# Kernel optimization log

Measured on AMD Instinct MI355X. Metric: run time of the kernel, lower is better.

The kernel has to match this reference:

```python
import jax, jax.numpy as jnp
import numpy as np

N = 8192
NFEAT = 512
NHID = 256
NCLASS = 40
EDGE_P = 0.002  # ~16 avg degree


def setup_inputs() -> dict:
    key = jax.random.key(0)
    k1, k2, k3, k4 = jax.random.split(key, 4)
    x = jax.random.normal(k1, (N, NFEAT), dtype=jnp.float32)
    # unnormalized binary adjacency without self loops (module adds eye itself)
    adj = (jax.random.uniform(k2, (N, N)) < EDGE_P).astype(jnp.float32)
    # GCNConv weights: torch.rand(in, out) -> uniform[0,1)
    W1 = jax.random.uniform(k3, (NFEAT, NHID), dtype=jnp.float32)
    W2 = jax.random.uniform(k4, (NHID, NCLASS), dtype=jnp.float32)
    return {"x": x, "adj": adj, "W1": W1, "W2": W2}


def reference(x, adj, W1, W2):
    n = adj.shape[0]
    # add self loops: in_adj.to_dense() + eye
    A_hat = adj + jnp.eye(n, dtype=adj.dtype)
    # normalize_adj: D^{-1/2} A_hat D^{-1/2} (diag matmuls == row/col scaling)
    d = A_hat.sum(-1) ** -0.5  # [N]
    norm_adj = d[:, None] * A_hat * d[None, :]
    # conv1: relu(adj @ x @ W1); dropout is identity in eval mode
    h = jax.nn.relu((norm_adj @ x) @ W1)
    # conv2 reuses the same normalized adjacency (only one DGG layer by default)
    h2 = jax.nn.relu((norm_adj @ h) @ W2)
    return jax.nn.log_softmax(h2, axis=-1)
```

## Files before the change

### kernel.cpp

```cpp
#include <hip/hip_runtime.h>
#include <math.h>

#define NV 8192
#define CAP 64

__global__ __launch_bounds__(256) void build_graph(
    const float* __restrict__ adj, int* __restrict__ cols,
    int* __restrict__ rowcount, float* __restrict__ dinv,
    float* __restrict__ diagv) {
  int row = blockIdx.x;
  int t = threadIdx.x;
  __shared__ int cnt;
  __shared__ float sdiag;
  __shared__ float ssum[256];
  if (t == 0) { cnt = 0; sdiag = 0.0f; }
  __syncthreads();
  const float4* arow = (const float4*)(adj + (size_t)row * NV);
  float s = 0.0f;
  for (int i = t; i < NV / 4; i += 256) {
    float4 v = arow[i];
    s += v.x + v.y + v.z + v.w;
    int c0 = i * 4;
    if (v.x != 0.0f) { if (c0 + 0 == row) sdiag = v.x; else { int p = atomicAdd(&cnt, 1); if (p < CAP) cols[(size_t)row * CAP + p] = c0 + 0; } }
    if (v.y != 0.0f) { if (c0 + 1 == row) sdiag = v.y; else { int p = atomicAdd(&cnt, 1); if (p < CAP) cols[(size_t)row * CAP + p] = c0 + 1; } }
    if (v.z != 0.0f) { if (c0 + 2 == row) sdiag = v.z; else { int p = atomicAdd(&cnt, 1); if (p < CAP) cols[(size_t)row * CAP + p] = c0 + 2; } }
    if (v.w != 0.0f) { if (c0 + 3 == row) sdiag = v.w; else { int p = atomicAdd(&cnt, 1); if (p < CAP) cols[(size_t)row * CAP + p] = c0 + 3; } }
  }
  ssum[t] = s;
  __syncthreads();
  for (int off = 128; off > 0; off >>= 1) {
    if (t < off) ssum[t] += ssum[t + off];
    __syncthreads();
  }
  if (t == 0) {
    float deg = ssum[0] + 1.0f;
    dinv[row] = 1.0f / sqrtf(deg);
    diagv[row] = sdiag + 1.0f;
    rowcount[row] = cnt > CAP ? CAP : cnt;
  }
}

__global__ __launch_bounds__(256) void gemm_f32(
    const float* __restrict__ A, const float* __restrict__ B,
    float* __restrict__ C, int M, int K, int Nvalid, int ldb, int ldc) {
  __shared__ float As[16][68];
  __shared__ float Bs[16][64];
  int t = threadIdx.x;
  int bm0 = blockIdx.y * 64;
  int bn0 = blockIdx.x * 64;
  int tx = t & 15, ty = t >> 4;
  int ar = t >> 2;
  int ak = (t & 3) * 4;
  int bk = t >> 4;
  int bn = (t & 15) * 4;
  float acc[4][4] = {};
  for (int k0 = 0; k0 < K; k0 += 16) {
    float4 av = *(const float4*)(A + (size_t)(bm0 + ar) * K + k0 + ak);
    float4 bv;
    int bc = bn0 + bn;
    if (bc + 3 < Nvalid) {
      bv = *(const float4*)(B + (size_t)(k0 + bk) * ldb + bc);
    } else {
      bv.x = (bc + 0 < Nvalid) ? B[(size_t)(k0 + bk) * ldb + bc + 0] : 0.0f;
      bv.y = (bc + 1 < Nvalid) ? B[(size_t)(k0 + bk) * ldb + bc + 1] : 0.0f;
      bv.z = (bc + 2 < Nvalid) ? B[(size_t)(k0 + bk) * ldb + bc + 2] : 0.0f;
      bv.w = (bc + 3 < Nvalid) ? B[(size_t)(k0 + bk) * ldb + bc + 3] : 0.0f;
    }
    As[ak + 0][ar] = av.x;
    As[ak + 1][ar] = av.y;
    As[ak + 2][ar] = av.z;
    As[ak + 3][ar] = av.w;
    *(float4*)(&Bs[bk][bn]) = bv;
    __syncthreads();
#pragma unroll
    for (int kk = 0; kk < 16; kk++) {
      float4 a = *(const float4*)(&As[kk][ty * 4]);
      float4 b = *(const float4*)(&Bs[kk][tx * 4]);
      acc[0][0] += a.x * b.x; acc[0][1] += a.x * b.y; acc[0][2] += a.x * b.z; acc[0][3] += a.x * b.w;
      acc[1][0] += a.y * b.x; acc[1][1] += a.y * b.y; acc[1][2] += a.y * b.z; acc[1][3] += a.y * b.w;
      acc[2][0] += a.z * b.x; acc[2][1] += a.z * b.y; acc[2][2] += a.z * b.z; acc[2][3] += a.z * b.w;
      acc[3][0] += a.w * b.x; acc[3][1] += a.w * b.y; acc[3][2] += a.w * b.z; acc[3][3] += a.w * b.w;
    }
    __syncthreads();
  }
#pragma unroll
  for (int i = 0; i < 4; i++) {
    *(float4*)(C + (size_t)(bm0 + ty * 4 + i) * ldc + bn0 + tx * 4) =
        make_float4(acc[i][0], acc[i][1], acc[i][2], acc[i][3]);
  }
}

__global__ __launch_bounds__(256) void spmm_relu_k(
    const float* __restrict__ Z, const int* __restrict__ cols,
    const int* __restrict__ rowcount, const float* __restrict__ dinv,
    const float* __restrict__ diagv, float* __restrict__ H) {
  int row = blockIdx.x;
  int f = threadIdx.x;
  float di = dinv[row];
  float acc = diagv[row] * di * Z[(size_t)row * 256 + f];
  int cnt = rowcount[row];
  const int* cr = cols + (size_t)row * CAP;
  for (int e = 0; e < cnt; e++) {
    int c = cr[e];
    acc += dinv[c] * Z[(size_t)c * 256 + f];
  }
  H[(size_t)row * 256 + f] = fmaxf(acc * di, 0.0f);
}

__global__ __launch_bounds__(256) void spmm2_lsm_k(
    const float* __restrict__ Z, const int* __restrict__ cols,
    const int* __restrict__ rowcount, const float* __restrict__ dinv,
    const float* __restrict__ diagv, float* __restrict__ out) {
  int lane = threadIdx.x & 63;
  int row = blockIdx.x * 4 + (threadIdx.x >> 6);
  float di = dinv[row];
  float acc = 0.0f;
  if (lane < 40) acc = diagv[row] * di * Z[(size_t)row * 64 + lane];
  int cnt = rowcount[row];
  const int* cr = cols + (size_t)row * CAP;
  for (int e = 0; e < cnt; e++) {
    int c = cr[e];
    if (lane < 40) acc += dinv[c] * Z[(size_t)c * 64 + lane];
  }
  float h2 = (lane < 40) ? fmaxf(acc * di, 0.0f) : -INFINITY;
  float m = h2;
  for (int off = 32; off > 0; off >>= 1) m = fmaxf(m, __shfl_xor(m, off, 64));
  float ex = (lane < 40) ? expf(h2 - m) : 0.0f;
  float s = ex;
  for (int off = 32; off > 0; off >>= 1) s += __shfl_xor(s, off, 64);
  float ls = logf(s);
  if (lane < 40) out[(size_t)row * 40 + lane] = h2 - m - ls;
}

extern "C" void kernel_launch(void* const* d_in, const int* in_sizes, int n_in,
                              void* d_out, int out_size, void* d_ws, size_t ws_size,
                              hipStream_t stream) {
  (void)in_sizes; (void)n_in; (void)out_size; (void)ws_size;
  const float* x   = (const float*)d_in[0];
  const float* adj = (const float*)d_in[1];
  const float* W1  = (const float*)d_in[2];
  const float* W2  = (const float*)d_in[3];
  float* out = (float*)d_out;
  char* ws = (char*)d_ws;

  int*   cols     = (int*)(ws);
  int*   rowcount = (int*)(ws + 2097152);
  float* dinv     = (float*)(ws + 2097152 + 32768);
  float* diagv    = (float*)(ws + 2097152 + 65536);
  float* XW1      = (float*)(ws + 2097152 + 98304);
  float* H        = (float*)(ws + 2097152 + 98304 + 8388608);
  float* HW2      = (float*)(ws + 2097152 + 98304 + 16777216);

  hipLaunchKernelGGL(build_graph, dim3(NV), dim3(256), 0, stream,
                     adj, cols, rowcount, dinv, diagv);
  hipLaunchKernelGGL(gemm_f32, dim3(4, 128), dim3(256), 0, stream,
                     x, W1, XW1, NV, 512, 256, 256, 256);
  hipLaunchKernelGGL(spmm_relu_k, dim3(NV), dim3(256), 0, stream,
                     XW1, cols, rowcount, dinv, diagv, H);
  hipLaunchKernelGGL(gemm_f32, dim3(1, 128), dim3(256), 0, stream,
                     H, W2, HW2, NV, 256, 40, 40, 64);
  hipLaunchKernelGGL(spmm2_lsm_k, dim3(NV / 4), dim3(256), 0, stream,
                     HW2, cols, rowcount, dinv, diagv, out);
}
```

Measured before the change: 473.7 us.

## Use wave ballot compaction in graph build and vectorize SpMM gathers

The graph-build kernel replaces per-element shared atomics with wave-level ballot/popcount compaction and counts nonzeros as integers instead of a float tree reduction. It assumes a binary adjacency, so the diagonal value becomes 2 or 1. The first SpMM now processes one row per wave with float4 loads and a 4-way unrolled gather, and the second SpMM gets the same unroll with the lane<40 predicate removed. The aim is to cut atomic contention in the dominant adjacency scan and raise memory-level parallelism in the gathers. The cost is a binary-adjacency assumption and reads of padding columns of HW2.

```diff
diff --git a/kernel.cpp b/kernel.cpp
--- a/kernel.cpp
+++ b/kernel.cpp
@@ -10,32 +10,48 @@
     float* __restrict__ diagv) {
   int row = blockIdx.x;
   int t = threadIdx.x;
+  int lane = t & 63;
   __shared__ int cnt;
-  __shared__ float sdiag;
-  __shared__ float ssum[256];
-  if (t == 0) { cnt = 0; sdiag = 0.0f; }
+  __shared__ int diag_nz;
+  __shared__ int wsum[4];
+  if (t == 0) { cnt = 0; diag_nz = 0; }
   __syncthreads();
   const float4* arow = (const float4*)(adj + (size_t)row * NV);
-  float s = 0.0f;
+  int mycount = 0;
   for (int i = t; i < NV / 4; i += 256) {
     float4 v = arow[i];
-    s += v.x + v.y + v.z + v.w;
-    int c0 = i * 4;
-    if (v.x != 0.0f) { if (c0 + 0 == row) sdiag = v.x; else { int p = atomicAdd(&cnt, 1); if (p < CAP) cols[(size_t)row * CAP + p] = c0 + 0; } }
-    if (v.y != 0.0f) { if (c0 + 1 == row) sdiag = v.y; else { int p = atomicAdd(&cnt, 1); if (p < CAP) cols[(size_t)row * CAP + p] = c0 + 1; } }
-    if (v.z != 0.0f) { if (c0 + 2 == row) sdiag = v.z; else { int p = atomicAdd(&cnt, 1); if (p < CAP) cols[(size_t)row * CAP + p] = c0 + 2; } }
-    if (v.w != 0.0f) { if (c0 + 3 == row) sdiag = v.w; else { int p = atomicAdd(&cnt, 1); if (p < CAP) cols[(size_t)row * CAP + p] = c0 + 3; } }
-  }
-  ssum[t] = s;
+    float va[4] = {v.x, v.y, v.z, v.w};
+#pragma unroll
+    for (int j = 0; j < 4; j++) {
+      bool nz = (va[j] != 0.0f);
+      mycount += nz ? 1 : 0;
+      int c = i * 4 + j;
+      bool isdiag = nz && (c == row);
+      bool take = nz && !isdiag;
+      if (isdiag) diag_nz = 1;
+      unsigned long long m = __ballot(take);
+      if (m != 0ull) {
+        int tot = __popcll(m);
+        int pre = __popcll(m & ((1ull << lane) - 1ull));
+        int leader = __ffsll((unsigned long long)m) - 1;
+        int base = 0;
+        if (lane == leader) base = atomicAdd(&cnt, tot);
+        base = __shfl(base, leader, 64);
+        if (take) {
+          int p = base + pre;
+          if (p < CAP) cols[(size_t)row * CAP + p] = c;
+        }
+      }
+    }
+  }
+  for (int off = 32; off > 0; off >>= 1) mycount += __shfl_xor(mycount, off, 64);
+  if (lane == 0) wsum[t >> 6] = mycount;
   __syncthreads();
-  for (int off = 128; off > 0; off >>= 1) {
-    if (t < off) ssum[t] += ssum[t + off];
-    __syncthreads();
-  }
   if (t == 0) {
-    float deg = ssum[0] + 1.0f;
+    int nnz = wsum[0] + wsum[1] + wsum[2] + wsum[3];
+    float deg = (float)nnz + 1.0f;
     dinv[row] = 1.0f / sqrtf(deg);
-    diagv[row] = sdiag + 1.0f;
+    diagv[row] = diag_nz ? 2.0f : 1.0f;
     rowcount[row] = cnt > CAP ? CAP : cnt;
   }
 }
@@ -94,17 +110,41 @@
     const float* __restrict__ Z, const int* __restrict__ cols,
     const int* __restrict__ rowcount, const float* __restrict__ dinv,
     const float* __restrict__ diagv, float* __restrict__ H) {
-  int row = blockIdx.x;
-  int f = threadIdx.x;
+  int lane = threadIdx.x & 63;
+  int row = blockIdx.x * 4 + (threadIdx.x >> 6);
+  const float4* Zr = (const float4*)Z;
   float di = dinv[row];
-  float acc = diagv[row] * di * Z[(size_t)row * 256 + f];
+  float4 z = Zr[(size_t)row * 64 + lane];
+  float dd = diagv[row] * di;
+  float4 acc;
+  acc.x = dd * z.x; acc.y = dd * z.y; acc.z = dd * z.z; acc.w = dd * z.w;
   int cnt = rowcount[row];
   const int* cr = cols + (size_t)row * CAP;
-  for (int e = 0; e < cnt; e++) {
+  int e = 0;
+  for (; e + 4 <= cnt; e += 4) {
+    int c0 = cr[e + 0], c1 = cr[e + 1], c2 = cr[e + 2], c3 = cr[e + 3];
+    float w0 = dinv[c0], w1 = dinv[c1], w2 = dinv[c2], w3 = dinv[c3];
+    float4 g0 = Zr[(size_t)c0 * 64 + lane];
+    float4 g1 = Zr[(size_t)c1 * 64 + lane];
+    float4 g2 = Zr[(size_t)c2 * 64 + lane];
+    float4 g3 = Zr[(size_t)c3 * 64 + lane];
+    acc.x += w0 * g0.x + w1 * g1.x + w2 * g2.x + w3 * g3.x;
+    acc.y += w0 * g0.y + w1 * g1.y + w2 * g2.y + w3 * g3.y;
+    acc.z += w0 * g0.z + w1 * g1.z + w2 * g2.z + w3 * g3.z;
+    acc.w += w0 * g0.w + w1 * g1.w + w2 * g2.w + w3 * g3.w;
+  }
+  for (; e < cnt; e++) {
     int c = cr[e];
-    acc += dinv[c] * Z[(size_t)c * 256 + f];
-  }
-  H[(size_t)row * 256 + f] = fmaxf(acc * di, 0.0f);
+    float w = dinv[c];
+    float4 g = Zr[(size_t)c * 64 + lane];
+    acc.x += w * g.x; acc.y += w * g.y; acc.z += w * g.z; acc.w += w * g.w;
+  }
+  float4 o;
+  o.x = fmaxf(acc.x * di, 0.0f);
+  o.y = fmaxf(acc.y * di, 0.0f);
+  o.z = fmaxf(acc.z * di, 0.0f);
+  o.w = fmaxf(acc.w * di, 0.0f);
+  ((float4*)H)[(size_t)row * 64 + lane] = o;
 }
 
 __global__ __launch_bounds__(256) void spmm2_lsm_k(
@@ -114,13 +154,22 @@
   int lane = threadIdx.x & 63;
   int row = blockIdx.x * 4 + (threadIdx.x >> 6);
   float di = dinv[row];
-  float acc = 0.0f;
-  if (lane < 40) acc = diagv[row] * di * Z[(size_t)row * 64 + lane];
+  float acc = diagv[row] * di * Z[(size_t)row * 64 + lane];
   int cnt = rowcount[row];
   const int* cr = cols + (size_t)row * CAP;
-  for (int e = 0; e < cnt; e++) {
+  int e = 0;
+  for (; e + 4 <= cnt; e += 4) {
+    int c0 = cr[e + 0], c1 = cr[e + 1], c2 = cr[e + 2], c3 = cr[e + 3];
+    float w0 = dinv[c0], w1 = dinv[c1], w2 = dinv[c2], w3 = dinv[c3];
+    float g0 = Z[(size_t)c0 * 64 + lane];
+    float g1 = Z[(size_t)c1 * 64 + lane];
+    float g2 = Z[(size_t)c2 * 64 + lane];
+    float g3 = Z[(size_t)c3 * 64 + lane];
+    acc += w0 * g0 + w1 * g1 + w2 * g2 + w3 * g3;
+  }
+  for (; e < cnt; e++) {
     int c = cr[e];
-    if (lane < 40) acc += dinv[c] * Z[(size_t)c * 64 + lane];
+    acc += dinv[c] * Z[(size_t)c * 64 + lane];
   }
   float h2 = (lane < 40) ? fmaxf(acc * di, 0.0f) : -INFINITY;
   float m = h2;
@@ -145,17 +194,17 @@
 
   int*   cols     = (int*)(ws);
   int*   rowcount = (int*)(ws + 2097152);
-  float* dinv     = (float*)(ws + 2097152 + 32768);
-  float* diagv    = (float*)(ws + 2097152 + 65536);
-  float* XW1      = (float*)(ws + 2097152 + 98304);
-  float* H        = (float*)(ws + 2097152 + 98304 + 8388608);
-  float* HW2      = (float*)(ws + 2097152 + 98304 + 16777216);
+  float* dinv     = (float*)(ws + 2129920);
+  float* diagv    = (float*)(ws + 2162688);
+  float* XW1      = (float*)(ws + 2195456);
+  float* H        = (float*)(ws + 10584064);
+  float* HW2      = (float*)(ws + 18972672);
 
   hipLaunchKernelGGL(build_graph, dim3(NV), dim3(256), 0, stream,
                      adj, cols, rowcount, dinv, diagv);
   hipLaunchKernelGGL(gemm_f32, dim3(4, 128), dim3(256), 0, stream,
                      x, W1, XW1, NV, 512, 256, 256, 256);
-  hipLaunchKernelGGL(spmm_relu_k, dim3(NV), dim3(256), 0, stream,
+  hipLaunchKernelGGL(spmm_relu_k, dim3(NV / 4), dim3(256), 0, stream,
                      XW1, cols, rowcount, dinv, diagv, H);
   hipLaunchKernelGGL(gemm_f32, dim3(1, 128), dim3(256), 0, stream,
                      H, W2, HW2, NV, 256, 40, 40, 64);
```

Result: faster. 451.4 us (-4.7%).
